# Kernel tuning notes

Measured on AMD Instinct MI355X. Metric: run time of the kernel, lower is better.

## Reference

```python
import jax, jax.numpy as jnp
import numpy as np

B, N, H = 4, 200, 300


def setup_inputs() -> dict:
    key = jax.random.key(0)
    ks = jax.random.split(key, 6)
    s = 1.0 / np.sqrt(H)
    return {
        "x": jax.random.normal(ks[0], (B, N, H), dtype=jnp.float32),
        "e": jax.random.normal(ks[1], (B, N, N, H), dtype=jnp.float32),
        "U_w": jax.random.uniform(ks[2], (H, H), jnp.float32, -s, s),
        "U_b": jax.random.uniform(ks[3], (H,), jnp.float32, -s, s),
        "V_w": jax.random.uniform(ks[4], (H, H), jnp.float32, -s, s),
        "V_b": jax.random.uniform(ks[5], (H,), jnp.float32, -s, s),
    }


def reference(x, e, U_w, U_b, V_w, V_b):
    # Ue = e @ U_w.T + U_b  -> (B, N, N, H)
    Ue = jnp.einsum("bijh,gh->bijg", e, U_w) + U_b
    # Vx = x @ V_w.T + V_b  -> (B, N, H)
    Vx = jnp.einsum("bnh,gh->bng", x, V_w) + V_b
    # e_new[b,i,j] = Ue[b,i,j] + Vx[b,i] + Vx[b,j]
    e_new = Ue + Vx[:, :, None, :] + Vx[:, None, :, :]
    return e_new
```

## Files before the change

### kernel.cpp

```cpp
#include <hip/hip_runtime.h>
#include <hip/hip_bf16.h>

#define BB 4
#define NN 200
#define HH 300
#define KSN 10
#define GF 20
#define BM 128
#define NCHUNK 5
#define BCHUNK 40960

typedef __attribute__((ext_vector_type(8))) short short8;
typedef __attribute__((ext_vector_type(4))) float float4v;

static __device__ __forceinline__ ushort f2bf(float x) {
    union { float f; uint u; } v; v.f = x;
    uint r = v.u + 0x7FFFu + ((v.u >> 16) & 1u);
    return (ushort)(r >> 16);
}

static __device__ __forceinline__ short8 pack8_cvt(float4v a, float4v b) {
    uint u0, u1, u2, u3;
    asm("v_cvt_pk_bf16_f32 %0, %1, %2" : "=v"(u0) : "v"(a[0]), "v"(a[1]));
    asm("v_cvt_pk_bf16_f32 %0, %1, %2" : "=v"(u1) : "v"(a[2]), "v"(a[3]));
    asm("v_cvt_pk_bf16_f32 %0, %1, %2" : "=v"(u2) : "v"(b[0]), "v"(b[1]));
    asm("v_cvt_pk_bf16_f32 %0, %1, %2" : "=v"(u3) : "v"(b[2]), "v"(b[3]));
    union { uint u[4]; short8 s; } r;
    r.u[0] = u0; r.u[1] = u1; r.u[2] = u2; r.u[3] = u3;
    return r.s;
}

static __device__ __forceinline__ void gload_lds16(const void* g, void* l) {
    __builtin_amdgcn_global_load_lds(
        (const __attribute__((address_space(1))) unsigned int*)g,
        (__attribute__((address_space(3))) unsigned int*)l, 16, 0, 0);
}

__global__ void pack_u(const float* __restrict__ Uw, ushort* __restrict__ Bp) {
    int idx = blockIdx.x * 256 + threadIdx.x;
    if (idx >= KSN * GF * 64) return;
    int lane = idx & 63;
    int kg = idx >> 6;
    int gf = kg % GF, ks = kg / GF;
    int g = gf * 16 + (lane & 15);
    int h0 = ks * 32 + (lane >> 4) * 8;
    ushort v[8];
#pragma unroll
    for (int j = 0; j < 8; ++j) {
        int h = h0 + j;
        v[j] = (g < HH && h < HH) ? f2bf(Uw[g * HH + h]) : (ushort)0;
    }
    *reinterpret_cast<short8*>(Bp + (size_t)idx * 8) = *reinterpret_cast<const short8*>(v);
}

__global__ void vx_kernel(const float* __restrict__ x, const float* __restrict__ Vw,
                          const float* __restrict__ Vb, const float* __restrict__ Ub,
                          float* __restrict__ Vx) {
    __shared__ float xs[HH];
    int row = blockIdx.x;
    const float* xr = x + (size_t)row * HH;
    for (int h = threadIdx.x; h < HH; h += 256) xs[h] = xr[h];
    __syncthreads();
    for (int g = threadIdx.x; g < HH; g += 256) {
        const float4* wr = reinterpret_cast<const float4*>(Vw + (size_t)g * HH);
        const float4* xv = reinterpret_cast<const float4*>(xs);
        float s0 = 0.f, s1 = 0.f, s2 = 0.f, s3 = 0.f;
#pragma unroll 5
        for (int k = 0; k < HH / 4; ++k) {
            float4 w = wr[k];
            float4 xx = xv[k];
            s0 += w.x * xx.x; s1 += w.y * xx.y; s2 += w.z * xx.z; s3 += w.w * xx.w;
        }
        Vx[(size_t)row * HH + g] = Vb[g] + 0.5f * Ub[g] + s0 + s1 + s2 + s3;
    }
}

__launch_bounds__(512, 2)
__global__ void gemm_kernel(const float* __restrict__ e, const ushort* __restrict__ Bp,
                            const float* __restrict__ Vx, float* __restrict__ out) {
    __shared__ float  Af[2][BM][64];
    __shared__ ushort Bf[2][BCHUNK / 2];
    const int tid = threadIdx.x;
    const int w = tid >> 6, l = tid & 63;
    const int r = l & 15, q = l >> 4;
    const int m0 = blockIdx.x * BM;

#define WAITV(N_) asm volatile("s_waitcnt vmcnt(" #N_ ")" ::: "memory")
#define BAR() do {                                                   \
        __builtin_amdgcn_sched_barrier(0);                           \
        asm volatile("s_waitcnt lgkmcnt(0)" ::: "memory");           \
        __builtin_amdgcn_sched_barrier(0);                           \
        __builtin_amdgcn_s_barrier();                                \
        __builtin_amdgcn_sched_barrier(0);                           \
    } while (0)

#define STAGE_A(KC_, P_) do {                                                   \
        _Pragma("unroll")                                                       \
        for (int rd_ = 0; rd_ < 4; ++rd_) {                                     \
            int row_ = rd_ * 32 + w * 4 + (l >> 4);                             \
            int ucl_ = (l & 15) ^ (row_ & 15);                                  \
            const char* src_ = (const char*)(e + (size_t)(m0 + row_) * HH)      \
                               + (KC_) * 256 + ucl_ * 16;                       \
            if ((KC_) == 4 && ucl_ >= 11) src_ = (const char*)e;                \
            gload_lds16(src_, (char*)&Af[P_][0][0] + rd_ * 8192 + w * 1024 + l * 16); \
        }                                                                       \
    } while (0)

#define STAGE_B(KC_, P_) do {                                                   \
        const char* bs_ = (const char*)Bp + (size_t)(KC_) * BCHUNK;             \
        char* bd_ = (char*)&Bf[P_][0];                                          \
        _Pragma("unroll")                                                       \
        for (int rd_ = 0; rd_ < 5; ++rd_)                                       \
            gload_lds16(bs_ + rd_ * 8192 + tid * 16, bd_ + rd_ * 8192 + tid * 16); \
    } while (0)

    float4v acc[GF];
#pragma unroll
    for (int f = 0; f < GF; ++f) acc[f] = (float4v){0.f, 0.f, 0.f, 0.f};

#define COMPUTE(P_) do {                                                        \
        const char* ab_ = (const char*)&Af[P_][0][0] + (w * 16 + r) * 256;      \
        const ushort* bb_ = &Bf[P_][0];                                         \
        _Pragma("unroll")                                                       \
        for (int s_ = 0; s_ < 2; ++s_) {                                        \
            int u0_ = (s_ * 8 + 2 * q) ^ r;                                     \
            int u1_ = (s_ * 8 + 2 * q + 1) ^ r;                                 \
            float4v fa0_ = *reinterpret_cast<const float4v*>(ab_ + u0_ * 16);   \
            float4v fa1_ = *reinterpret_cast<const float4v*>(ab_ + u1_ * 16);   \
            short8 fa_ = pack8_cvt(fa0_, fa1_);                                 \
            const ushort* bs_ = bb_ + s_ * (GF * 512) + l * 8;                  \
            _Pragma("unroll")                                                   \
            for (int f_ = 0; f_ < GF; ++f_) {                                   \
                short8 bfr_ = *reinterpret_cast<const short8*>(bs_ + f_ * 512); \
                acc[f_] = __builtin_amdgcn_mfma_f32_16x16x32_bf16(bfr_, fa_, acc[f_], 0, 0, 0); \
            }                                                                   \
        }                                                                       \
    } while (0)

    STAGE_A(0, 0); STAGE_B(0, 0);
    STAGE_A(1, 1); STAGE_B(1, 1);
    WAITV(9); BAR();

    COMPUTE(0); BAR();
    STAGE_A(2, 0); STAGE_B(2, 0); WAITV(9); BAR();

    COMPUTE(1); BAR();
    STAGE_A(3, 1); STAGE_B(3, 1); WAITV(9); BAR();

    COMPUTE(0); BAR();
    STAGE_A(4, 0); STAGE_B(4, 0); WAITV(9); BAR();

    COMPUTE(1); BAR();
    WAITV(0); BAR();

    COMPUTE(0);

    {
        const int mrow = m0 + w * 16 + r;
        int j = mrow % NN;
        int ti = mrow / NN;
        int b = ti / NN;
        const float* vi = Vx + (size_t)ti * HH;
        const float* vj = Vx + (size_t)(b * NN + j) * HH;
        float* orow = out + (size_t)mrow * HH;
#pragma unroll
        for (int f = 0; f < GF - 1; ++f) {
            int g0 = f * 16 + q * 4;
            if (g0 + 4 <= HH) {
                float4v vi4 = *reinterpret_cast<const float4v*>(vi + g0);
                float4v vj4 = *reinterpret_cast<const float4v*>(vj + g0);
                *reinterpret_cast<float4v*>(orow + g0) = acc[f] + vi4 + vj4;
            }
        }
    }
#undef COMPUTE
#undef STAGE_A
#undef STAGE_B
#undef BAR
#undef WAITV
}

extern "C" void kernel_launch(void* const* d_in, const int* in_sizes, int n_in,
                              void* d_out, int out_size, void* d_ws, size_t ws_size,
                              hipStream_t stream) {
    const float* x  = (const float*)d_in[0];
    const float* e  = (const float*)d_in[1];
    const float* Uw = (const float*)d_in[2];
    const float* Ub = (const float*)d_in[3];
    const float* Vw = (const float*)d_in[4];
    const float* Vb = (const float*)d_in[5];
    float* out = (float*)d_out;

    ushort* Bp = (ushort*)d_ws;
    float*  Vx = (float*)((char*)d_ws + 204800);

    pack_u<<<50, 256, 0, stream>>>(Uw, Bp);
    vx_kernel<<<BB * NN, 256, 0, stream>>>(x, Vw, Vb, Ub, Vx);
    gemm_kernel<<<160000 / BM, 512, 0, stream>>>(e, Bp, Vx, out);
}
```

Before: 153.0 us.

## Stage A through registers with bf16 conversion before LDS, smaller tiles, deeper pipeline

The GEMM kernel now loads e rows into registers, converts them to bf16, and writes packed fragments to LDS, instead of DMAing fp32 into LDS and converting inside the compute loop. The tile shrinks to 64 rows and 256 threads with a 10-step K pipeline of 32 columns each, with register prefetch three steps ahead. This halves LDS footprint and removes per-MFMA conversion work, allowing 3 blocks per CU. The cost is more barriers and register pressure, plus a weaker async overlap for A because register loads must wait before each LDS write.

```diff
diff --git a/kernel.cpp b/kernel.cpp
--- a/kernel.cpp
+++ b/kernel.cpp
@@ -4,11 +4,9 @@
 #define BB 4
 #define NN 200
 #define HH 300
-#define KSN 10
+#define NCH 10
 #define GF 20
-#define BM 128
-#define NCHUNK 5
-#define BCHUNK 40960
+#define BM 64
 
 typedef __attribute__((ext_vector_type(8))) short short8;
 typedef __attribute__((ext_vector_type(4))) float float4v;
@@ -38,7 +36,7 @@
 
 __global__ void pack_u(const float* __restrict__ Uw, ushort* __restrict__ Bp) {
     int idx = blockIdx.x * 256 + threadIdx.x;
-    if (idx >= KSN * GF * 64) return;
+    if (idx >= NCH * GF * 64) return;
     int lane = idx & 63;
     int kg = idx >> 6;
     int gf = kg % GF, ks = kg / GF;
@@ -75,85 +73,89 @@
     }
 }
 
-__launch_bounds__(512, 2)
+__launch_bounds__(256, 3)
 __global__ void gemm_kernel(const float* __restrict__ e, const ushort* __restrict__ Bp,
                             const float* __restrict__ Vx, float* __restrict__ out) {
-    __shared__ float  Af[2][BM][64];
-    __shared__ ushort Bf[2][BCHUNK / 2];
+    __shared__ __align__(16) ushort Alds[2][BM * 32];
+    __shared__ __align__(16) ushort Blds[2][GF * 512];
     const int tid = threadIdx.x;
     const int w = tid >> 6, l = tid & 63;
     const int r = l & 15, q = l >> 4;
     const int m0 = blockIdx.x * BM;
-
-#define WAITV(N_) asm volatile("s_waitcnt vmcnt(" #N_ ")" ::: "memory")
-#define BAR() do {                                                   \
-        __builtin_amdgcn_sched_barrier(0);                           \
-        asm volatile("s_waitcnt lgkmcnt(0)" ::: "memory");           \
-        __builtin_amdgcn_sched_barrier(0);                           \
-        __builtin_amdgcn_s_barrier();                                \
-        __builtin_amdgcn_sched_barrier(0);                           \
-    } while (0)
-
-#define STAGE_A(KC_, P_) do {                                                   \
-        _Pragma("unroll")                                                       \
-        for (int rd_ = 0; rd_ < 4; ++rd_) {                                     \
-            int row_ = rd_ * 32 + w * 4 + (l >> 4);                             \
-            int ucl_ = (l & 15) ^ (row_ & 15);                                  \
-            const char* src_ = (const char*)(e + (size_t)(m0 + row_) * HH)      \
-                               + (KC_) * 256 + ucl_ * 16;                       \
-            if ((KC_) == 4 && ucl_ >= 11) src_ = (const char*)e;                \
-            gload_lds16(src_, (char*)&Af[P_][0][0] + rd_ * 8192 + w * 1024 + l * 16); \
-        }                                                                       \
-    } while (0)
-
-#define STAGE_B(KC_, P_) do {                                                   \
-        const char* bs_ = (const char*)Bp + (size_t)(KC_) * BCHUNK;             \
-        char* bd_ = (char*)&Bf[P_][0];                                          \
-        _Pragma("unroll")                                                       \
-        for (int rd_ = 0; rd_ < 5; ++rd_)                                       \
-            gload_lds16(bs_ + rd_ * 8192 + tid * 16, bd_ + rd_ * 8192 + tid * 16); \
-    } while (0)
+    const int arow = tid >> 2;
+    const int acg = tid & 3;
+    const float* rowp = e + (size_t)(m0 + arow) * HH;
+    const int awidx = ((arow >> 4) * 64 + (arow & 15) + acg * 16) * 8;
+
+    float4v s0a, s0b, s1a, s1b, s2a, s2b;
 
     float4v acc[GF];
 #pragma unroll
     for (int f = 0; f < GF; ++f) acc[f] = (float4v){0.f, 0.f, 0.f, 0.f};
 
+#define LOAD_A(K_, S_) do {                                                     \
+        int c0_ = (K_) * 32 + acg * 8;                                          \
+        const float* p0_ = (c0_ + 4 <= HH) ? rowp + c0_ : e;                    \
+        const float* p1_ = (c0_ + 8 <= HH) ? rowp + c0_ + 4 : e;                \
+        S_##a = *reinterpret_cast<const float4v*>(p0_);                         \
+        S_##b = *reinterpret_cast<const float4v*>(p1_);                         \
+    } while (0)
+
+#define WRITE_A(K_, S_, P_) do {                                                \
+        short8 w_ = pack8_cvt(S_##a, S_##b);                                    \
+        if ((K_) == 9) {                                                        \
+            _Pragma("unroll")                                                   \
+            for (int j_ = 0; j_ < 8; ++j_)                                      \
+                if (288 + acg * 8 + j_ >= HH) w_[j_] = 0;                       \
+        }                                                                       \
+        *reinterpret_cast<short8*>(&Alds[P_][awidx]) = w_;                      \
+    } while (0)
+
+#define ISSUE_B(K_, P_) do {                                                    \
+        const char* bs_ = (const char*)Bp + (size_t)(K_) * (GF * 1024);         \
+        char* bd_ = (char*)&Blds[P_][0];                                        \
+        _Pragma("unroll")                                                       \
+        for (int rd_ = 0; rd_ < 5; ++rd_)                                       \
+            gload_lds16(bs_ + rd_ * 4096 + tid * 16, bd_ + rd_ * 4096 + tid * 16); \
+    } while (0)
+
 #define COMPUTE(P_) do {                                                        \
-        const char* ab_ = (const char*)&Af[P_][0][0] + (w * 16 + r) * 256;      \
-        const ushort* bb_ = &Bf[P_][0];                                         \
+        short8 fa_ = *reinterpret_cast<const short8*>(&Alds[P_][(w * 64 + l) * 8]); \
+        const ushort* bb_ = &Blds[P_][l * 8];                                   \
         _Pragma("unroll")                                                       \
-        for (int s_ = 0; s_ < 2; ++s_) {                                        \
-            int u0_ = (s_ * 8 + 2 * q) ^ r;                                     \
-            int u1_ = (s_ * 8 + 2 * q + 1) ^ r;                                 \
-            float4v fa0_ = *reinterpret_cast<const float4v*>(ab_ + u0_ * 16);   \
-            float4v fa1_ = *reinterpret_cast<const float4v*>(ab_ + u1_ * 16);   \
-            short8 fa_ = pack8_cvt(fa0_, fa1_);                                 \
-            const ushort* bs_ = bb_ + s_ * (GF * 512) + l * 8;                  \
-            _Pragma("unroll")                                                   \
-            for (int f_ = 0; f_ < GF; ++f_) {                                   \
-                short8 bfr_ = *reinterpret_cast<const short8*>(bs_ + f_ * 512); \
-                acc[f_] = __builtin_amdgcn_mfma_f32_16x16x32_bf16(bfr_, fa_, acc[f_], 0, 0, 0); \
-            }                                                                   \
+        for (int f_ = 0; f_ < GF; ++f_) {                                       \
+            short8 bf_ = *reinterpret_cast<const short8*>(bb_ + f_ * 512);      \
+            acc[f_] = __builtin_amdgcn_mfma_f32_16x16x32_bf16(bf_, fa_, acc[f_], 0, 0, 0); \
         }                                                                       \
     } while (0)
 
-    STAGE_A(0, 0); STAGE_B(0, 0);
-    STAGE_A(1, 1); STAGE_B(1, 1);
-    WAITV(9); BAR();
-
-    COMPUTE(0); BAR();
-    STAGE_A(2, 0); STAGE_B(2, 0); WAITV(9); BAR();
-
-    COMPUTE(1); BAR();
-    STAGE_A(3, 1); STAGE_B(3, 1); WAITV(9); BAR();
-
-    COMPUTE(0); BAR();
-    STAGE_A(4, 0); STAGE_B(4, 0); WAITV(9); BAR();
-
-    COMPUTE(1); BAR();
-    WAITV(0); BAR();
-
-    COMPUTE(0);
+#define WAITV(N_) do {                                                          \
+        __builtin_amdgcn_sched_barrier(0);                                      \
+        asm volatile("s_waitcnt vmcnt(" #N_ ")" ::: "memory");                  \
+        __builtin_amdgcn_sched_barrier(0);                                      \
+    } while (0)
+
+#define ENDPHASE() do {                                                         \
+        asm volatile("s_waitcnt lgkmcnt(0)" ::: "memory");                      \
+        __builtin_amdgcn_s_barrier();                                           \
+        __builtin_amdgcn_sched_barrier(0);                                      \
+    } while (0)
+
+    LOAD_A(0, s0); ISSUE_B(0, 0); LOAD_A(1, s1); LOAD_A(2, s2);
+    WRITE_A(0, s0, 0);
+    WAITV(2);
+    ENDPHASE();
+
+    WRITE_A(1, s1, 1); ISSUE_B(1, 1); LOAD_A(3, s0); COMPUTE(0); WAITV(2); ENDPHASE();
+    WRITE_A(2, s2, 0); ISSUE_B(2, 0); LOAD_A(4, s1); COMPUTE(1); WAITV(2); ENDPHASE();
+    WRITE_A(3, s0, 1); ISSUE_B(3, 1); LOAD_A(5, s2); COMPUTE(0); WAITV(2); ENDPHASE();
+    WRITE_A(4, s1, 0); ISSUE_B(4, 0); LOAD_A(6, s0); COMPUTE(1); WAITV(2); ENDPHASE();
+    WRITE_A(5, s2, 1); ISSUE_B(5, 1); LOAD_A(7, s1); COMPUTE(0); WAITV(2); ENDPHASE();
+    WRITE_A(6, s0, 0); ISSUE_B(6, 0); LOAD_A(8, s2); COMPUTE(1); WAITV(2); ENDPHASE();
+    WRITE_A(7, s1, 1); ISSUE_B(7, 1); LOAD_A(9, s0); COMPUTE(0); WAITV(2); ENDPHASE();
+    WRITE_A(8, s2, 0); ISSUE_B(8, 0);                COMPUTE(1); WAITV(0); ENDPHASE();
+    WRITE_A(9, s0, 1); ISSUE_B(9, 1);                COMPUTE(0); WAITV(0); ENDPHASE();
+    COMPUTE(1);
 
     {
         const int mrow = m0 + w * 16 + r;
@@ -173,11 +175,12 @@
             }
         }
     }
+#undef LOAD_A
+#undef WRITE_A
+#undef ISSUE_B
 #undef COMPUTE
-#undef STAGE_A
-#undef STAGE_B
-#undef BAR
 #undef WAITV
+#undef ENDPHASE
 }
 
 extern "C" void kernel_launch(void* const* d_in, const int* in_sizes, int n_in,
@@ -196,5 +199,5 @@
 
     pack_u<<<50, 256, 0, stream>>>(Uw, Bp);
     vx_kernel<<<BB * NN, 256, 0, stream>>>(x, Vw, Vb, Ub, Vx);
-    gemm_kernel<<<160000 / BM, 512, 0, stream>>>(e, Bp, Vx, out);
-}
+    gemm_kernel<<<160000 / BM, 256, 0, stream>>>(e, Bp, Vx, out);
+}
```

After: 166.3 us. 1.09x slower.
